# Kernel optimization log

Hardware: AMD Instinct MI355X
Metric: run time of the kernel (lower is better)

Reference implementation:

```python
import jax, jax.numpy as jnp
import numpy as np

B, N, M = 32, 32, 64          # batch, timesteps, local group length (group_token_length+3)
NL, NG = 192, 768             # n_embd_local, n_embd_global
HL, HG = 6, 12                # n_head_local, n_head_global


def setup_inputs() -> dict:
    key = jax.random.key(0)
    ks = jax.random.split(key, 16)
    def w(k, shape, s=0.02):
        return jax.random.normal(k, shape, jnp.float32) * s
    inp = {}
    inp["xl"] = jax.random.normal(ks[0], (B, N, M, NL), jnp.float32)
    inp["xg"] = jax.random.normal(ks[1], (B, 2 * N, NG), jnp.float32)
    i = 2
    for pre, d in (("l", NL), ("g", NG)):
        inp[f"{pre}_ln1_w"] = jnp.ones((d,), jnp.float32)
        inp[f"{pre}_ln1_b"] = jnp.zeros((d,), jnp.float32)
        inp[f"{pre}_ln2_w"] = jnp.ones((d,), jnp.float32)
        inp[f"{pre}_ln2_b"] = jnp.zeros((d,), jnp.float32)
        for nm in ("q", "k", "v", "o"):
            inp[f"{pre}_w{nm}"] = w(ks[i], (d, d)); i += 1
            inp[f"{pre}_b{nm}"] = jnp.zeros((d,), jnp.float32)
        inp[f"{pre}_w1"] = w(ks[i], (d, 4 * d)); i += 1
        inp[f"{pre}_b1"] = jnp.zeros((4 * d,), jnp.float32)
        inp[f"{pre}_w2"] = w(ks[i], (4 * d, d)); i += 1
        inp[f"{pre}_b2"] = jnp.zeros((d,), jnp.float32)
    inp["d_w"] = w(ks[i], (M * NL, NG))
    inp["d_b"] = jnp.zeros((NG,), jnp.float32)
    return inp


def _ln(x, g, b):
    m = x.mean(-1, keepdims=True)
    v = ((x - m) ** 2).mean(-1, keepdims=True)
    return (x - m) / jnp.sqrt(v + 1e-5) * g + b


def _attn(x, wq, bq, wk, bk, wv, bv, wo, bo, nh, allow):
    # x: [B', L, D]; allow: [L, L] bool (True = attend)
    Bx, L, D = x.shape
    hd = D // nh
    q = (x @ wq + bq).reshape(Bx, L, nh, hd)
    k = (x @ wk + bk).reshape(Bx, L, nh, hd)
    v = (x @ wv + bv).reshape(Bx, L, nh, hd)
    s = jnp.einsum('bihd,bjhd->bhij', q, k) / np.float32(np.sqrt(hd))
    s = jnp.where(allow[None, None], s, -jnp.inf)
    p = jax.nn.softmax(s, axis=-1)
    y = jnp.einsum('bhij,bjhd->bihd', p, v).reshape(Bx, L, D)
    return y @ wo + bo


def _tblock(x, p, nh, allow):
    (ln1w, ln1b, ln2w, ln2b, wq, bq, wk, bk, wv, bv, wo, bo, w1, b1, w2, b2) = p
    x = x + _attn(_ln(x, ln1w, ln1b), wq, bq, wk, bk, wv, bv, wo, bo, nh, allow)
    h = _ln(x, ln2w, ln2b)
    return x + (jax.nn.gelu(h @ w1 + b1, approximate=False) @ w2 + b2)


def reference(xl, xg,
              l_ln1_w, l_ln1_b, l_ln2_w, l_ln2_b,
              l_wq, l_bq, l_wk, l_bk, l_wv, l_bv, l_wo, l_bo,
              l_w1, l_b1, l_w2, l_b2,
              g_ln1_w, g_ln1_b, g_ln2_w, g_ln2_b,
              g_wq, g_bq, g_wk, g_bk, g_wv, g_bv, g_wo, g_bo,
              g_w1, g_b1, g_w2, g_b2,
              d_w, d_b):
    Bx, Nx, Mx, nl = xl.shape
    ng = xg.shape[-1]
    lp = (l_ln1_w, l_ln1_b, l_ln2_w, l_ln2_b, l_wq, l_bq, l_wk, l_bk,
          l_wv, l_bv, l_wo, l_bo, l_w1, l_b1, l_w2, l_b2)
    gp = (g_ln1_w, g_ln1_b, g_ln2_w, g_ln2_b, g_wq, g_bq, g_wk, g_bk,
          g_wv, g_bv, g_wo, g_bo, g_w1, g_b1, g_w2, g_b2)

    # local block: causal attention within each group of M tokens
    allow_l = jnp.tril(jnp.ones((Mx, Mx), bool))
    x = _tblock(xl.reshape(Bx * Nx, Mx, nl), lp, HL, allow_l)
    xl_out = x.reshape(Bx, Nx, Mx, nl)

    # summarize each group into one global token, interleave with xg pairs
    zg = (xl_out.reshape(Bx, Nx, Mx * nl) @ d_w + d_b)[:, :, None, :]  # [B,N,1,ng]
    zg = jnp.concatenate([zg, xg.reshape(Bx, Nx, 2, ng)], axis=2)      # [B,N,3,ng]
    zg = zg.reshape(Bx, 3 * Nx, ng)

    # global mask: tril plus within-triplet upper entries; the global block
    # additionally applies its own causal mask, so combined = causal & custom
    L = 3 * Nx
    idx = jnp.arange(L)
    causal = idx[:, None] >= idx[None, :]
    custom = causal | (idx[:, None] // 3 == idx[None, :] // 3)
    allow_g = causal & custom

    zg = _tblock(zg, gp, HG, allow_g)
    xg_out = zg.reshape(Bx, Nx, 3, ng)[:, :, 1:, :].reshape(Bx, 2 * Nx, ng)
    return (xl_out, xg_out)
```

## Files before the change

### kernel.cpp

```cpp
#include <hip/hip_runtime.h>
#include <hip/hip_bf16.h>


typedef unsigned short ushort;
typedef __bf16 bf16x8 __attribute__((ext_vector_type(8)));
typedef float f32x4 __attribute__((ext_vector_type(4)));

__device__ __forceinline__ ushort f2us(float f) {
  __hip_bfloat16 h = __float2bfloat16(f);
  return *reinterpret_cast<ushort*>(&h);
}
__device__ __forceinline__ float gelu_exact(float v) {
  return 0.5f * v * (1.f + erff(v * 0.70710678118654752f));
}
__device__ __forceinline__ void gload16(const ushort* g, ushort* l) {
  __builtin_amdgcn_global_load_lds(
      (const __attribute__((address_space(1))) void*)g,
      (__attribute__((address_space(3))) void*)l, 16, 0, 0);
}

struct TJobs { const float* s[13]; ushort* d[13]; };

__global__ __launch_bounds__(256)
void transp_all(TJobs J)
{
  static constexpr int NN[13]  = {192,192,192,192,768,192,768,768,768,768,768,3072,768};
  static constexpr int SS[13]  = {192,192,192,192,192,768,12288,768,768,768,768,768,3072};
  static constexpr int RO[13]  = {0,192,384,0,0,0,0,0,768,1536,0,0,0};
  static constexpr int CUM[14] = {0,9,18,27,36,72,108,2412,2556,2700,2844,2988,3564,4140};
  __shared__ float t[64][65];
  int bid = blockIdx.x;
  int j = 0;
  while (bid >= CUM[j + 1]) ++j;
  int tIdx = bid - CUM[j];
  const int N = NN[j], stride = SS[j], rowOff = RO[j];
  const int nx = N >> 6;
  const int n0 = (tIdx % nx) * 64, k0 = (tIdx / nx) * 64;
  const float* W = J.s[j];
  ushort* Wt = J.d[j];
  int c = threadIdx.x & 63, r = threadIdx.x >> 6;
  #pragma unroll
  for (int i = 0; i < 16; ++i) {
    int kr = r + i * 4;
    t[kr][c] = W[(size_t)(k0 + kr) * N + n0 + c];
  }
  __syncthreads();
  #pragma unroll
  for (int i = 0; i < 16; ++i) {
    int nr = r + i * 4;
    Wt[(size_t)(rowOff + n0 + nr) * stride + k0 + c] = f2us(t[c][nr]);
  }
}

__global__ __launch_bounds__(256)
void pack3_kernel(float* dst, const float* a, int na, const float* b, int nb,
                  const float* c, int nc)
{
  int i = blockIdx.x * 256 + threadIdx.x;
  if (i >= na + nb + nc) return;
  dst[i] = (i < na) ? a[i] : (i < na + nb ? b[i - na] : c[i - na - nb]);
}

template<int D>
__global__ __launch_bounds__(256)
void ln_kernel(const float* __restrict__ x, const float* __restrict__ g,
               const float* __restrict__ bb, ushort* __restrict__ out, int rows)
{
  int wave = threadIdx.x >> 6, lane = threadIdx.x & 63;
  int row = blockIdx.x * 4 + wave;
  if (row >= rows) return;
  const float* xr = x + (size_t)row * D;
  constexpr int E = D / 64;
  float vals[E];
  float s = 0.f;
  #pragma unroll
  for (int e = 0; e < E; ++e) { vals[e] = xr[e * 64 + lane]; s += vals[e]; }
  #pragma unroll
  for (int off = 32; off >= 1; off >>= 1) s += __shfl_xor(s, off);
  float m = s * (1.f / D);
  float s2 = 0.f;
  #pragma unroll
  for (int e = 0; e < E; ++e) { float d = vals[e] - m; s2 += d * d; }
  #pragma unroll
  for (int off = 32; off >= 1; off >>= 1) s2 += __shfl_xor(s2, off);
  float rstd = rsqrtf(s2 * (1.f / D) + 1e-5f);
  ushort* orow = out + (size_t)row * D;
  #pragma unroll
  for (int e = 0; e < E; ++e) {
    int c = e * 64 + lane;
    orow[c] = f2us((vals[e] - m) * rstd * g[c] + bb[c]);
  }
}

template<int ACT, int RES, int OUTF, int OUTB, int BIAS>
__global__ __launch_bounds__(256)
void mgemm(const ushort* __restrict__ A, const ushort* __restrict__ Bt,
           const float* __restrict__ bias, const float* __restrict__ resF,
           float* __restrict__ Cf, ushort* __restrict__ Cb,
           int M, int N, int K)
{
  __shared__ __align__(16) ushort Asm[128 * 32];
  __shared__ __align__(16) ushort Bsm[64 * 32];
  const int tid = threadIdx.x;
  const int wave = tid >> 6, lane = tid & 63;
  const int quad = lane >> 4, lm = lane & 15;
  const int rowBase = blockIdx.y * 128, colBase = blockIdx.x * 64;
  const int wrow = (wave & 1) * 64, wcol = (wave >> 1) * 32;
  const int srow = lane >> 2, skcol = (lane & 3) * 8;

  f32x4 acc[4][2] = {};
  for (int k0 = 0; k0 < K; k0 += 32) {
    #pragma unroll
    for (int uu = 0; uu < 3; ++uu) {
      int u = wave * 3 + uu;
      if (u < 8) {
        const ushort* gp = A + (size_t)(rowBase + u * 16 + srow) * K + k0 + skcol;
        gload16(gp, &Asm[u * 512]);
      } else {
        int v = u - 8;
        const ushort* gp = Bt + (size_t)(colBase + v * 16 + srow) * K + k0 + skcol;
        gload16(gp, &Bsm[v * 512]);
      }
    }
    __syncthreads();
    bf16x8 af[4], bfr[2];
    #pragma unroll
    for (int r2 = 0; r2 < 4; ++r2)
      af[r2] = *reinterpret_cast<const bf16x8*>(&Asm[(wrow + r2 * 16 + lm) * 32 + quad * 8]);
    #pragma unroll
    for (int c2 = 0; c2 < 2; ++c2)
      bfr[c2] = *reinterpret_cast<const bf16x8*>(&Bsm[(wcol + c2 * 16 + lm) * 32 + quad * 8]);
    #pragma unroll
    for (int r2 = 0; r2 < 4; ++r2)
      #pragma unroll
      for (int c2 = 0; c2 < 2; ++c2)
        acc[r2][c2] = __builtin_amdgcn_mfma_f32_16x16x32_bf16(af[r2], bfr[c2], acc[r2][c2], 0, 0, 0);
    __syncthreads();
  }

  #pragma unroll
  for (int r2 = 0; r2 < 4; ++r2) {
    #pragma unroll
    for (int c2 = 0; c2 < 2; ++c2) {
      int col = colBase + wcol + c2 * 16 + lm;
      int row0 = rowBase + wrow + r2 * 16 + quad * 4;
      #pragma unroll
      for (int g = 0; g < 4; ++g) {
        float v = acc[r2][c2][g];
        size_t idx = (size_t)(row0 + g) * N + col;
        if (BIAS) v += bias[col];
        if (ACT == 1) v = gelu_exact(v);
        if (RES) v += resF[idx];
        if (OUTF) Cf[idx] = v;
        if (OUTB) Cb[idx] = f2us(v);
      }
    }
  }
}

template<int ACT, int RES, int OUTF, int OUTB, int BIAS, int SPLITK>
__global__ __launch_bounds__(256)
void mgemm128(const ushort* __restrict__ A, const ushort* __restrict__ Bt,
              const float* __restrict__ bias, const float* __restrict__ resF,
              float* __restrict__ Cf, ushort* __restrict__ Cb,
              int M, int N, int K, int kChunk)
{
  __shared__ __align__(16) ushort Asm[128 * 32];
  __shared__ __align__(16) ushort Bsm[128 * 32];
  const int tid = threadIdx.x;
  const int wave = tid >> 6, lane = tid & 63;
  const int quad = lane >> 4, lm = lane & 15;
  const int rowBase = blockIdx.y * 128, colBase = blockIdx.x * 128;
  const int wrow = (wave & 1) * 64, wcol = (wave >> 1) * 64;
  const int srow = lane >> 2, skcol = (lane & 3) * 8;

  f32x4 acc[4][4] = {};
  const int kbeg = SPLITK ? blockIdx.z * kChunk : 0;
  const int kend = kbeg + (SPLITK ? kChunk : K);

  for (int k0 = kbeg; k0 < kend; k0 += 32) {
    #pragma unroll
    for (int uu = 0; uu < 4; ++uu) {
      int u = wave * 4 + uu;
      if (u < 8) {
        const ushort* gp = A + (size_t)(rowBase + u * 16 + srow) * K + k0 + skcol;
        gload16(gp, &Asm[u * 512]);
      } else {
        int v = u - 8;
        const ushort* gp = Bt + (size_t)(colBase + v * 16 + srow) * K + k0 + skcol;
        gload16(gp, &Bsm[v * 512]);
      }
    }
    __syncthreads();
    bf16x8 af[4], bfr[4];
    #pragma unroll
    for (int r2 = 0; r2 < 4; ++r2)
      af[r2] = *reinterpret_cast<const bf16x8*>(&Asm[(wrow + r2 * 16 + lm) * 32 + quad * 8]);
    #pragma unroll
    for (int c2 = 0; c2 < 4; ++c2)
      bfr[c2] = *reinterpret_cast<const bf16x8*>(&Bsm[(wcol + c2 * 16 + lm) * 32 + quad * 8]);
    #pragma unroll
    for (int r2 = 0; r2 < 4; ++r2)
      #pragma unroll
      for (int c2 = 0; c2 < 4; ++c2)
        acc[r2][c2] = __builtin_amdgcn_mfma_f32_16x16x32_bf16(af[r2], bfr[c2], acc[r2][c2], 0, 0, 0);
    __syncthreads();
  }

  const size_t zoff = SPLITK ? (size_t)blockIdx.z * M * N : 0;
  #pragma unroll
  for (int r2 = 0; r2 < 4; ++r2) {
    #pragma unroll
    for (int c2 = 0; c2 < 4; ++c2) {
      int col = colBase + wcol + c2 * 16 + lm;
      int row0 = rowBase + wrow + r2 * 16 + quad * 4;
      #pragma unroll
      for (int g = 0; g < 4; ++g) {
        float v = acc[r2][c2][g];
        size_t idx = (size_t)(row0 + g) * N + col;
        if (BIAS) v += bias[col];
        if (ACT == 1) v = gelu_exact(v);
        if (RES) v += resF[idx];
        if (OUTF) Cf[zoff + idx] = v;
        if (OUTB) Cb[idx] = f2us(v);
      }
    }
  }
}

__global__ __launch_bounds__(256)
void reduce8_kernel(const float* __restrict__ P, const float* __restrict__ db,
                    float* __restrict__ ZG)
{
  int i = blockIdx.x * 256 + threadIdx.x;
  float s = db[i % 768];
  #pragma unroll
  for (int k = 0; k < 8; ++k) s += P[i + k * 786432];
  ZG[i] = s;
}

__global__ __launch_bounds__(256)
void reduce4res_kernel(const float* __restrict__ P, const float* __restrict__ db,
                       const float* __restrict__ res, float* __restrict__ out)
{
  int i = blockIdx.x * 256 + threadIdx.x;
  float s = db[i % 768] + res[i];
  #pragma unroll
  for (int k = 0; k < 4; ++k) s += P[i + k * 2359296];
  out[i] = s;
}

template<int L, int HD, int NW>
__global__ __launch_bounds__(NW * 64)
void fattn(const ushort* __restrict__ QKV, ushort* __restrict__ Yp,
           int nh, int DS, int DY, int offQ, int offK, int offV)
{
  constexpr int PQ = HD + 8;
  constexpr int PV = L + 8;
  constexpr int KS = HD / 32;
  constexpr int NCT = L / 16;
  constexpr int KS2 = L / 32;
  constexpr int NYT = HD / 16;
  constexpr int T = NW * 64;
  __shared__ __align__(16) ushort Ql[L * PQ];
  __shared__ __align__(16) ushort Kl[L * PQ];
  __shared__ __align__(16) ushort Vt[HD * PV];
  __shared__ __align__(16) ushort Ps[L * PV];
  const int tid = threadIdx.x;
  const int b = blockIdx.x / nh, h = blockIdx.x % nh;
  const size_t rowb = (size_t)b * L * DS;
  const int hb = h * HD;
  constexpr int CH = L * HD / 8;
  for (int idx = tid; idx < CH; idx += T) {
    int row = idx / (HD / 8), seg = idx % (HD / 8);
    uint4 q4 = *reinterpret_cast<const uint4*>(&QKV[rowb + (size_t)row * DS + offQ + hb + seg * 8]);
    *reinterpret_cast<uint4*>(&Ql[row * PQ + seg * 8]) = q4;
    uint4 k4 = *reinterpret_cast<const uint4*>(&QKV[rowb + (size_t)row * DS + offK + hb + seg * 8]);
    *reinterpret_cast<uint4*>(&Kl[row * PQ + seg * 8]) = k4;
  }
  for (int idx = tid; idx < L * HD; idx += T) {
    int j = idx / HD, d = idx % HD;
    Vt[d * PV + j] = QKV[rowb + (size_t)j * DS + offV + hb + d];
  }
  __syncthreads();
  const int lane = tid & 63;
  const int quad = lane >> 4, lm = lane & 15;
  const int rt = tid >> 6;
  const float scale = rsqrtf((float)HD);
  bf16x8 af[KS];
  #pragma unroll
  for (int s = 0; s < KS; ++s)
    af[s] = *reinterpret_cast<const bf16x8*>(&Ql[(rt * 16 + lm) * PQ + s * 32 + quad * 8]);
  f32x4 sacc[NCT] = {};
  #pragma unroll
  for (int ct = 0; ct < NCT; ++ct)
    #pragma unroll
    for (int s = 0; s < KS; ++s) {
      bf16x8 bf = *reinterpret_cast<const bf16x8*>(&Kl[(ct * 16 + lm) * PQ + s * 32 + quad * 8]);
      sacc[ct] = __builtin_amdgcn_mfma_f32_16x16x32_bf16(af[s], bf, sacc[ct], 0, 0, 0);
    }
  float inv[4];
  #pragma unroll
  for (int g = 0; g < 4; ++g) {
    const int row = rt * 16 + quad * 4 + g;
    float sv[NCT]; float m = -1e30f;
    #pragma unroll
    for (int ct = 0; ct < NCT; ++ct) {
      int col = ct * 16 + lm;
      float x = sacc[ct][g] * scale;
      sv[ct] = (col <= row) ? x : -1e30f;
      m = fmaxf(m, sv[ct]);
    }
    #pragma unroll
    for (int off = 8; off >= 1; off >>= 1) m = fmaxf(m, __shfl_xor(m, off));
    float l = 0.f;
    #pragma unroll
    for (int ct = 0; ct < NCT; ++ct) {
      float p = __expf(sv[ct] - m);
      l += p;
      Ps[row * PV + ct * 16 + lm] = f2us(p);
    }
    #pragma unroll
    for (int off = 8; off >= 1; off >>= 1) l += __shfl_xor(l, off);
    inv[g] = 1.f / l;
  }
  __syncthreads();
  f32x4 yacc[NYT] = {};
  #pragma unroll
  for (int s = 0; s < KS2; ++s) {
    bf16x8 ap = *reinterpret_cast<const bf16x8*>(&Ps[(rt * 16 + lm) * PV + s * 32 + quad * 8]);
    #pragma unroll
    for (int ct = 0; ct < NYT; ++ct) {
      bf16x8 bv = *reinterpret_cast<const bf16x8*>(&Vt[(ct * 16 + lm) * PV + s * 32 + quad * 8]);
      yacc[ct] = __builtin_amdgcn_mfma_f32_16x16x32_bf16(ap, bv, yacc[ct], 0, 0, 0);
    }
  }
  #pragma unroll
  for (int ct = 0; ct < NYT; ++ct)
    #pragma unroll
    for (int g = 0; g < 4; ++g) {
      int row = rt * 16 + quad * 4 + g;
      int d = ct * 16 + lm;
      Yp[((size_t)b * L + row) * DY + hb + d] = f2us(yacc[ct][g] * inv[g]);
    }
}

__global__ __launch_bounds__(256)
void interleave_kernel(const float* __restrict__ zg, const float* __restrict__ xg,
                       float* __restrict__ z)
{
  int idx = blockIdx.x * 256 + threadIdx.x;
  int c = idx % 768;
  int tok = idx / 768;
  int b = tok / 96, r = tok % 96;
  int n = r / 3, t = r % 3;
  z[idx] = (t == 0) ? zg[((size_t)b * 32 + n) * 768 + c]
                    : xg[((size_t)b * 64 + 2 * n + (t - 1)) * 768 + c];
}

__global__ __launch_bounds__(256)
void gather_kernel(const float* __restrict__ zfin, float* __restrict__ dst)
{
  int idx = blockIdx.x * 256 + threadIdx.x;
  int c = idx % 768;
  int t = (idx / 768) % 64;
  int b = idx / (768 * 64);
  int n = t >> 1, s = t & 1;
  dst[idx] = zfin[((size_t)b * 96 + 3 * n + 1 + s) * 768 + c];
}

extern "C" void kernel_launch(void* const* d_in, const int* in_sizes, int n_in,
                              void* d_out, int out_size, void* d_ws, size_t ws_size,
                              hipStream_t stream) {
  const float* xl = (const float*)d_in[0];
  const float* xg = (const float*)d_in[1];
  const float* l_ln1_w = (const float*)d_in[2];  const float* l_ln1_b = (const float*)d_in[3];
  const float* l_ln2_w = (const float*)d_in[4];  const float* l_ln2_b = (const float*)d_in[5];
  const float* l_wq = (const float*)d_in[6];     const float* l_bq = (const float*)d_in[7];
  const float* l_wk = (const float*)d_in[8];     const float* l_bk = (const float*)d_in[9];
  const float* l_wv = (const float*)d_in[10];    const float* l_bv = (const float*)d_in[11];
  const float* l_wo = (const float*)d_in[12];    const float* l_bo = (const float*)d_in[13];
  const float* l_w1 = (const float*)d_in[14];    const float* l_b1 = (const float*)d_in[15];
  const float* l_w2 = (const float*)d_in[16];    const float* l_b2 = (const float*)d_in[17];
  const float* g_ln1_w = (const float*)d_in[18]; const float* g_ln1_b = (const float*)d_in[19];
  const float* g_ln2_w = (const float*)d_in[20]; const float* g_ln2_b = (const float*)d_in[21];
  const float* g_wq = (const float*)d_in[22];    const float* g_bq = (const float*)d_in[23];
  const float* g_wk = (const float*)d_in[24];    const float* g_bk = (const float*)d_in[25];
  const float* g_wv = (const float*)d_in[26];    const float* g_bv = (const float*)d_in[27];
  const float* g_wo = (const float*)d_in[28];    const float* g_bo = (const float*)d_in[29];
  const float* g_w1 = (const float*)d_in[30];    const float* g_b1 = (const float*)d_in[31];
  const float* g_w2 = (const float*)d_in[32];    const float* g_b2 = (const float*)d_in[33];
  const float* dw   = (const float*)d_in[34];    const float* db   = (const float*)d_in[35];

  float* outL = (float*)d_out;
  float* outG = outL + 12582912;

  char* W = (char*)d_ws;
  ushort* A_bf   = (ushort*)(W + 0);
  ushort* QKVl   = (ushort*)(W + 25165824);
  ushort* HIDl   = (ushort*)(W + 25165824);
  ushort* XLb    = (ushort*)(W + 75497472);
  float*  X1     = (float*)(W + 100663296);
  ushort* wqkv_t = (ushort*)(W + 150994944);
  ushort* wo_t   = (ushort*)(W + 151216128);
  ushort* w1_t   = (ushort*)(W + 151289856);
  ushort* w2_t   = (ushort*)(W + 151584768);
  ushort* wd_t   = (ushort*)(W + 151879680);
  ushort* wgqkv_t= (ushort*)(W + 170754048);
  ushort* wgo_t  = (ushort*)(W + 174292992);
  ushort* wg1_t  = (ushort*)(W + 175472640);
  ushort* wg2_t  = (ushort*)(W + 180191232);
  float*  bqkv_l = (float*)(W + 184909824);
  float*  bqkv_g = (float*)(W + 184912128);
  float*  ZGP  = (float*)(W + 0);
  float*  FC2P = (float*)(W + 0);
  float*  ZG   = (float*)(W + 25165824);
  float*  Z    = (float*)(W + 28311552);
  ushort* LNG  = (ushort*)(W + 37748736);
  ushort* QKVg = (ushort*)(W + 42467328);
  ushort* YG   = (ushort*)(W + 56623104);
  float*  X1G  = (float*)(W + 61341696);
  ushort* HLNG = (ushort*)(W + 70778880);
  ushort* HIDg = (ushort*)(W + 100663296);
  float*  OUTG = (float*)(W + 119537664);

  TJobs tj;
  tj.s[0] = l_wq; tj.s[1] = l_wk; tj.s[2] = l_wv; tj.s[3] = l_wo;
  tj.s[4] = l_w1; tj.s[5] = l_w2; tj.s[6] = dw;
  tj.s[7] = g_wq; tj.s[8] = g_wk; tj.s[9] = g_wv; tj.s[10] = g_wo;
  tj.s[11] = g_w1; tj.s[12] = g_w2;
  tj.d[0] = wqkv_t; tj.d[1] = wqkv_t; tj.d[2] = wqkv_t; tj.d[3] = wo_t;
  tj.d[4] = w1_t; tj.d[5] = w2_t; tj.d[6] = wd_t;
  tj.d[7] = wgqkv_t; tj.d[8] = wgqkv_t; tj.d[9] = wgqkv_t; tj.d[10] = wgo_t;
  tj.d[11] = wg1_t; tj.d[12] = wg2_t;
  transp_all<<<4140, 256, 0, stream>>>(tj);
  pack3_kernel<<<3, 256, 0, stream>>>(bqkv_l, l_bq, 192, l_bk, 192, l_bv, 192);
  pack3_kernel<<<9, 256, 0, stream>>>(bqkv_g, g_bq, 768, g_bk, 768, g_bv, 768);

  ln_kernel<192><<<16384, 256, 0, stream>>>(xl, l_ln1_w, l_ln1_b, A_bf, 65536);
  mgemm<0,0,0,1,1><<<dim3(9,512), 256, 0, stream>>>(A_bf, wqkv_t, bqkv_l, nullptr, nullptr, QKVl, 65536, 576, 192);
  fattn<64,32,4><<<6144, 256, 0, stream>>>(QKVl, A_bf, 6, 576, 192, 0, 192, 384);
  mgemm<0,1,1,0,1><<<dim3(3,512), 256, 0, stream>>>(A_bf, wo_t, l_bo, xl, X1, nullptr, 65536, 192, 192);
  ln_kernel<192><<<16384, 256, 0, stream>>>(X1, l_ln2_w, l_ln2_b, A_bf, 65536);
  for (int h = 0; h < 2; ++h) {
    size_t ro = (size_t)h * 32768 * 192;
    mgemm128<1,0,0,1,1,0><<<dim3(6,256), 256, 0, stream>>>(A_bf + ro, w1_t, l_b1, nullptr, nullptr, HIDl, 32768, 768, 192, 0);
    mgemm<0,1,1,1,1><<<dim3(3,256), 256, 0, stream>>>(HIDl, w2_t, l_b2, X1 + ro, outL + ro, XLb + ro, 32768, 192, 768);
  }
  mgemm128<0,0,1,0,0,1><<<dim3(6,8,8), 256, 0, stream>>>(XLb, wd_t, nullptr, nullptr, ZGP, nullptr, 1024, 768, 12288, 1536);
  reduce8_kernel<<<3072, 256, 0, stream>>>(ZGP, db, ZG);
  interleave_kernel<<<9216, 256, 0, stream>>>(ZG, xg, Z);
  ln_kernel<768><<<768, 256, 0, stream>>>(Z, g_ln1_w, g_ln1_b, LNG, 3072);
  mgemm128<0,0,0,1,1,0><<<dim3(18,24), 256, 0, stream>>>(LNG, wgqkv_t, bqkv_g, nullptr, nullptr, QKVg, 3072, 2304, 768, 0);
  fattn<96,64,6><<<384, 384, 0, stream>>>(QKVg, YG, 12, 2304, 768, 0, 768, 1536);
  mgemm<0,1,1,0,1><<<dim3(12,24), 256, 0, stream>>>(YG, wgo_t, g_bo, Z, X1G, nullptr, 3072, 768, 768);
  ln_kernel<768><<<768, 256, 0, stream>>>(X1G, g_ln2_w, g_ln2_b, HLNG, 3072);
  mgemm128<1,0,0,1,1,0><<<dim3(24,24), 256, 0, stream>>>(HLNG, wg1_t, g_b1, nullptr, nullptr, HIDg, 3072, 3072, 768, 0);
  mgemm128<0,0,1,0,0,1><<<dim3(6,24,4), 256, 0, stream>>>(HIDg, wg2_t, nullptr, nullptr, FC2P, nullptr, 3072, 768, 3072, 768);
  reduce4res_kernel<<<9216, 256, 0, stream>>>(FC2P, g_b2, X1G, OUTG);
  gather_kernel<<<6144, 256, 0, stream>>>(OUTG, outG);
}
```

Measured before the change: 693.1 us.

## Double-buffer LDS tiles in both MFMA GEMM kernels with async prefetch

Both GEMM kernels now keep two LDS buffers and issue global-to-LDS loads two K-steps ahead. Explicit vmcnt waits and barriers replace the per-iteration syncthreads, so MFMA work overlaps with the next tile loads. This doubles LDS use per block, which may lower occupancy. The vmcnt counts must match the number of loads each wave issues per stage.

```diff
diff --git a/kernel.cpp b/kernel.cpp
--- a/kernel.cpp
+++ b/kernel.cpp
@@ -99,43 +99,56 @@
            float* __restrict__ Cf, ushort* __restrict__ Cb,
            int M, int N, int K)
 {
-  __shared__ __align__(16) ushort Asm[128 * 32];
-  __shared__ __align__(16) ushort Bsm[64 * 32];
+  __shared__ __align__(16) ushort Asm[2][128 * 32];
+  __shared__ __align__(16) ushort Bsm[2][64 * 32];
   const int tid = threadIdx.x;
   const int wave = tid >> 6, lane = tid & 63;
   const int quad = lane >> 4, lm = lane & 15;
   const int rowBase = blockIdx.y * 128, colBase = blockIdx.x * 64;
   const int wrow = (wave & 1) * 64, wcol = (wave >> 1) * 32;
   const int srow = lane >> 2, skcol = (lane & 3) * 8;
-
-  f32x4 acc[4][2] = {};
-  for (int k0 = 0; k0 < K; k0 += 32) {
+  const int nIter = K >> 5;
+
+  auto stage = [&](int buf, int it) {
+    const int k0 = it * 32;
     #pragma unroll
     for (int uu = 0; uu < 3; ++uu) {
-      int u = wave * 3 + uu;
+      const int u = wave * 3 + uu;
       if (u < 8) {
         const ushort* gp = A + (size_t)(rowBase + u * 16 + srow) * K + k0 + skcol;
-        gload16(gp, &Asm[u * 512]);
+        gload16(gp, &Asm[buf][u * 512]);
       } else {
-        int v = u - 8;
+        const int v = u - 8;
         const ushort* gp = Bt + (size_t)(colBase + v * 16 + srow) * K + k0 + skcol;
-        gload16(gp, &Bsm[v * 512]);
+        gload16(gp, &Bsm[buf][v * 512]);
       }
     }
-    __syncthreads();
+  };
+
+  f32x4 acc[4][2] = {};
+  stage(0, 0);
+  if (nIter > 1) stage(1, 1);
+
+  for (int t = 0; t < nIter; ++t) {
+    const int cur = t & 1;
+    if (t + 1 < nIter) asm volatile("s_waitcnt vmcnt(3)" ::: "memory");
+    else               asm volatile("s_waitcnt vmcnt(0)" ::: "memory");
+    __builtin_amdgcn_s_barrier();
     bf16x8 af[4], bfr[2];
     #pragma unroll
     for (int r2 = 0; r2 < 4; ++r2)
-      af[r2] = *reinterpret_cast<const bf16x8*>(&Asm[(wrow + r2 * 16 + lm) * 32 + quad * 8]);
+      af[r2] = *reinterpret_cast<const bf16x8*>(&Asm[cur][(wrow + r2 * 16 + lm) * 32 + quad * 8]);
     #pragma unroll
     for (int c2 = 0; c2 < 2; ++c2)
-      bfr[c2] = *reinterpret_cast<const bf16x8*>(&Bsm[(wcol + c2 * 16 + lm) * 32 + quad * 8]);
+      bfr[c2] = *reinterpret_cast<const bf16x8*>(&Bsm[cur][(wcol + c2 * 16 + lm) * 32 + quad * 8]);
+    asm volatile("s_waitcnt lgkmcnt(0)" ::: "memory");
+    __builtin_amdgcn_s_barrier();
+    if (t + 2 < nIter) stage(cur, t + 2);
     #pragma unroll
     for (int r2 = 0; r2 < 4; ++r2)
       #pragma unroll
       for (int c2 = 0; c2 < 2; ++c2)
         acc[r2][c2] = __builtin_amdgcn_mfma_f32_16x16x32_bf16(af[r2], bfr[c2], acc[r2][c2], 0, 0, 0);
-    __syncthreads();
   }
 
   #pragma unroll
@@ -165,8 +178,8 @@
               float* __restrict__ Cf, ushort* __restrict__ Cb,
               int M, int N, int K, int kChunk)
 {
-  __shared__ __align__(16) ushort Asm[128 * 32];
-  __shared__ __align__(16) ushort Bsm[128 * 32];
+  __shared__ __align__(16) ushort Asm[2][128 * 32];
+  __shared__ __align__(16) ushort Bsm[2][128 * 32];
   const int tid = threadIdx.x;
   const int wave = tid >> 6, lane = tid & 63;
   const int quad = lane >> 4, lm = lane & 15;
@@ -174,37 +187,49 @@
   const int wrow = (wave & 1) * 64, wcol = (wave >> 1) * 64;
   const int srow = lane >> 2, skcol = (lane & 3) * 8;
 
-  f32x4 acc[4][4] = {};
   const int kbeg = SPLITK ? blockIdx.z * kChunk : 0;
-  const int kend = kbeg + (SPLITK ? kChunk : K);
-
-  for (int k0 = kbeg; k0 < kend; k0 += 32) {
+  const int nIter = (SPLITK ? kChunk : K) >> 5;
+
+  auto stage = [&](int buf, int it) {
+    const int k0 = kbeg + it * 32;
     #pragma unroll
     for (int uu = 0; uu < 4; ++uu) {
-      int u = wave * 4 + uu;
+      const int u = wave * 4 + uu;
       if (u < 8) {
         const ushort* gp = A + (size_t)(rowBase + u * 16 + srow) * K + k0 + skcol;
-        gload16(gp, &Asm[u * 512]);
+        gload16(gp, &Asm[buf][u * 512]);
       } else {
-        int v = u - 8;
+        const int v = u - 8;
         const ushort* gp = Bt + (size_t)(colBase + v * 16 + srow) * K + k0 + skcol;
-        gload16(gp, &Bsm[v * 512]);
+        gload16(gp, &Bsm[buf][v * 512]);
       }
     }
-    __syncthreads();
+  };
+
+  f32x4 acc[4][4] = {};
+  stage(0, 0);
+  if (nIter > 1) stage(1, 1);
+
+  for (int t = 0; t < nIter; ++t) {
+    const int cur = t & 1;
+    if (t + 1 < nIter) asm volatile("s_waitcnt vmcnt(4)" ::: "memory");
+    else               asm volatile("s_waitcnt vmcnt(0)" ::: "memory");
+    __builtin_amdgcn_s_barrier();
     bf16x8 af[4], bfr[4];
     #pragma unroll
     for (int r2 = 0; r2 < 4; ++r2)
-      af[r2] = *reinterpret_cast<const bf16x8*>(&Asm[(wrow + r2 * 16 + lm) * 32 + quad * 8]);
+      af[r2] = *reinterpret_cast<const bf16x8*>(&Asm[cur][(wrow + r2 * 16 + lm) * 32 + quad * 8]);
     #pragma unroll
     for (int c2 = 0; c2 < 4; ++c2)
-      bfr[c2] = *reinterpret_cast<const bf16x8*>(&Bsm[(wcol + c2 * 16 + lm) * 32 + quad * 8]);
+      bfr[c2] = *reinterpret_cast<const bf16x8*>(&Bsm[cur][(wcol + c2 * 16 + lm) * 32 + quad * 8]);
+    asm volatile("s_waitcnt lgkmcnt(0)" ::: "memory");
+    __builtin_amdgcn_s_barrier();
+    if (t + 2 < nIter) stage(cur, t + 2);
     #pragma unroll
     for (int r2 = 0; r2 < 4; ++r2)
       #pragma unroll
       for (int c2 = 0; c2 < 4; ++c2)
         acc[r2][c2] = __builtin_amdgcn_mfma_f32_16x16x32_bf16(af[r2], bfr[c2], acc[r2][c2], 0, 0, 0);
-    __syncthreads();
   }
 
   const size_t zoff = SPLITK ? (size_t)blockIdx.z * M * N : 0;
```

Measured after the change: 660.3 us. 4.7% less time.
